# Optimization experiments

Measured on AMD Instinct MI355X. Metric: run time of the kernel, lower is better.

The kernel has to match this reference:

```python
import jax, jax.numpy as jnp
import numpy as np

N_NODES = 100000


def gcn_conv(h_in, W, b, src, dst, ew, n_nodes):
    """PyG GCNConv: x' = D^{-1/2} (A + I) D^{-1/2} (x W) + b, with edge weights."""
    h = h_in @ W  # [N, F_out]
    loop = jnp.arange(n_nodes, dtype=src.dtype)
    row = jnp.concatenate([src, loop])            # sources (j)
    col = jnp.concatenate([dst, loop])            # targets (i)
    w = jnp.concatenate([ew, jnp.ones((n_nodes,), dtype=ew.dtype)])
    deg = jax.ops.segment_sum(w, col, num_segments=n_nodes)  # weighted in-degree incl. self-loops
    dinv = jnp.where(deg > 0, jax.lax.rsqrt(deg), 0.0)
    norm = dinv[row] * w * dinv[col]              # [E+N]
    msg = h[row] * norm[:, None]                  # gather + scale, [E+N, F_out]
    out = jax.ops.segment_sum(msg, col, num_segments=n_nodes)  # scatter to targets
    return out + b


def setup_inputs() -> dict:
    key = jax.random.key(0)
    k = jax.random.split(key, 6)
    N, E, F_in, F_hid = N_NODES, 3200000, 128, 64
    x = jax.random.normal(k[0], (N, F_in), dtype=jnp.float32)
    edge_index = jax.random.randint(k[1], (2, E), 0, N, dtype=jnp.int64)
    edge_weight = jax.random.uniform(k[2], (E,), dtype=jnp.float32)
    W1 = jax.random.normal(k[3], (F_in, F_hid), dtype=jnp.float32) * 0.1
    b1 = jnp.zeros((F_hid,), dtype=jnp.float32)
    W2 = jax.random.normal(k[4], (F_hid, 1), dtype=jnp.float32) * 0.1
    b2 = jnp.zeros((1,), dtype=jnp.float32)
    return {"x": x, "edge_index": edge_index, "edge_weight": edge_weight,
            "W1": W1, "b1": b1, "W2": W2, "b2": b2}


def reference(x, edge_index, edge_weight, W1, b1, W2, b2):
    n_nodes = x.shape[0]
    src, dst = edge_index[0], edge_index[1]
    h = jax.nn.relu(gcn_conv(x, W1, b1, src, dst, edge_weight, n_nodes))
    h = gcn_conv(h, W2, b2, src, dst, edge_weight, n_nodes)  # [N, 1]
    score = jax.nn.sigmoid(h)[:, 0]
    # degree-weighted scoring (original edges, no self-loops), scatter onto source
    deg_weighted = jax.ops.segment_sum(edge_weight, src, num_segments=n_nodes)
    deg_norm = deg_weighted / jnp.max(deg_weighted)
    return score * (1.0 + deg_norm)
```

## Files before the change

### kernel.cpp

```cpp
#include <hip/hip_runtime.h>
#include <hip/hip_fp16.h>
#include <math.h>

#define F_IN 128
#define F_HID 64
#define NWG 256
#define PT 1024
#define BSH 7
#define BSZ 128
#define BSHS 10
#define BSZS 1024
#define SEGCAP 6144

typedef float f32x2 __attribute__((ext_vector_type(2)));
typedef float f32x4 __attribute__((ext_vector_type(4)));
typedef __bf16 bf16x8 __attribute__((ext_vector_type(8)));

__device__ __forceinline__ unsigned char f32_to_fp8(float v) {
  unsigned r = __builtin_amdgcn_cvt_pk_fp8_f32(v, v, 0, false);
  return (unsigned char)(r & 0xFFu);
}

__device__ __forceinline__ __bf16 f32_bf16(float f) {
  unsigned u = __float_as_uint(f);
  unsigned r = (u + 0x7FFFu + ((u >> 16) & 1u)) >> 16;
  return __builtin_bit_cast(__bf16, (unsigned short)r);
}

__global__ void k_count(const int* __restrict__ src, const int* __restrict__ dst,
                        int* __restrict__ cntAll, int NBD, int NBS, int E) {
  extern __shared__ int sh[];
  int* hD = sh;
  int* hS = sh + NBD;
  int tid = threadIdx.x, w = blockIdx.x;
  for (int k = tid; k < NBD + NBS; k += PT) sh[k] = 0;
  __syncthreads();
  int C = (E + NWG - 1) / NWG;
  int e0 = w * C, e1 = min(E, e0 + C);
  for (int e = e0 + tid; e < e1; e += PT) {
    atomicAdd(&hD[dst[e] >> BSH], 1);
    atomicAdd(&hS[src[e] >> BSHS], 1);
  }
  __syncthreads();
  for (int b = tid; b < NBD; b += PT) cntAll[b * NWG + w] = hD[b];
  for (int b = tid; b < NBS; b += PT) cntAll[(NBD + b) * NWG + w] = hS[b];
}

__global__ void k_scanA(int* __restrict__ data, int* __restrict__ partials, int TOT) {
  __shared__ int lds[1024];
  int tid = threadIdx.x;
  int g = blockIdx.x * 1024 + tid;
  int v = (g < TOT) ? data[g] : 0;
  lds[tid] = v; __syncthreads();
  for (int o = 1; o < 1024; o <<= 1) {
    int t = (tid >= o) ? lds[tid - o] : 0;
    __syncthreads();
    lds[tid] += t;
    __syncthreads();
  }
  if (g < TOT) data[g] = lds[tid] - v;
  if (tid == 1023) partials[blockIdx.x] = lds[1023];
}

__global__ void k_scanB(int* partials, int nb, unsigned* maxbits) {
  __shared__ int lds[1024];
  int tid = threadIdx.x;
  if (tid == 0) *maxbits = 0u;
  int v = (tid < nb) ? partials[tid] : 0;
  lds[tid] = v; __syncthreads();
  for (int o = 1; o < 1024; o <<= 1) {
    int t = (tid >= o) ? lds[tid - o] : 0;
    __syncthreads();
    lds[tid] += t;
    __syncthreads();
  }
  if (tid < nb) partials[tid] = lds[tid] - v;
}

__global__ void k_scanC(int* __restrict__ data, const int* __restrict__ partials, int TOT) {
  int g = blockIdx.x * 1024 + threadIdx.x;
  if (g < TOT) data[g] += partials[g >> 10];
}

__global__ void k_part(const int* __restrict__ src, const int* __restrict__ dst,
                       const float* __restrict__ ew, const int* __restrict__ baseAll,
                       int2* __restrict__ gD, unsigned* __restrict__ gS,
                       int NBD, int NBS, int E) {
  extern __shared__ int sh[];
  int* cD = sh;
  int* cS = sh + NBD;
  int tid = threadIdx.x, w = blockIdx.x;
  for (int b = tid; b < NBD; b += PT) cD[b] = baseAll[b * NWG + w];
  for (int b = tid; b < NBS; b += PT) cS[b] = baseAll[(NBD + b) * NWG + w] - E;
  __syncthreads();
  int C = (E + NWG - 1) / NWG;
  int e0 = w * C, e1 = min(E, e0 + C);
  for (int e = e0 + tid; e < e1; e += PT) {
    int s = src[e], d = dst[e];
    float wv = ew[e];
    int pD = atomicAdd(&cD[d >> BSH], 1);
    gD[pD] = make_int2(s | ((d & (BSZ - 1)) << 24), __float_as_int(wv));
    int pS = atomicAdd(&cS[s >> BSHS], 1);
    unsigned hb = (unsigned)__half_as_ushort(__float2half(wv));
    gS[pS] = ((unsigned)(s & (BSZS - 1)) << 16) | hb;
  }
}

__global__ void k_csr(int2* __restrict__ gD, const int* __restrict__ baseAll,
                      int* __restrict__ off, float* __restrict__ dinv,
                      int NBD, int N, int E) {
  __shared__ int2 seg[SEGCAP];
  __shared__ int hist[BSZ];
  __shared__ int curs[BSZ];
  __shared__ float degf[BSZ];
  int tid = threadIdx.x, b = blockIdx.x;
  int bstart = baseAll[b * NWG];
  int bend = (b + 1 < NBD) ? baseAll[(b + 1) * NWG] : E;
  int cnt = bend - bstart;
  for (int k = tid; k < cnt; k += 256) seg[k] = gD[bstart + k];
  if (tid < BSZ) { hist[tid] = 0; degf[tid] = 0.f; }
  __syncthreads();
  for (int k = tid; k < cnt; k += 256) {
    int dl = seg[k].x >> 24;
    atomicAdd(&hist[dl], 1);
    atomicAdd(&degf[dl], __int_as_float(seg[k].y));
  }
  __syncthreads();
  int v = (tid < BSZ) ? hist[tid] : 0;
  for (int o = 1; o < BSZ; o <<= 1) {
    int t = (tid < BSZ && tid >= o) ? hist[tid - o] : 0;
    __syncthreads();
    if (tid < BSZ) hist[tid] += t;
    __syncthreads();
  }
  if (tid < BSZ) {
    int excl = hist[tid] - v;
    curs[tid] = excl;
    int node = b * BSZ + tid;
    if (node < N) {
      off[node] = bstart + excl;
      dinv[node] = rsqrtf(1.0f + degf[tid]);
    }
  }
  if (b == NBD - 1 && tid == 0) off[N] = E;
  __syncthreads();
  for (int k = tid; k < cnt; k += 256) {
    int2 ev = seg[k];
    int dl = ev.x >> 24;
    int slot = atomicAdd(&curs[dl], 1);
    gD[bstart + slot] = make_int2(ev.x & 0xFFFFFF, ev.y);
  }
}

__global__ void k_dw(const unsigned* __restrict__ gS, const int* __restrict__ baseAll,
                     float* __restrict__ dw, unsigned* maxbits,
                     int NBD, int NBS, int N, int E) {
  __shared__ float acc[BSZS];
  int tid = threadIdx.x, b = blockIdx.x;
  int bstart = baseAll[(NBD + b) * NWG] - E;
  int bend = (b + 1 < NBS) ? baseAll[(NBD + b + 1) * NWG] - E : E;
  acc[tid] = 0.f;
  __syncthreads();
  for (int k = bstart + tid; k < bend; k += BSZS) {
    unsigned p = gS[k];
    atomicAdd(&acc[p >> 16], __half2float(__ushort_as_half((unsigned short)(p & 0xFFFFu))));
  }
  __syncthreads();
  float m = 0.f;
  int node = b * BSZS + tid;
  if (node < N) { dw[node] = acc[tid]; m = acc[tid]; }
  for (int mm = 32; mm; mm >>= 1) m = fmaxf(m, __shfl_xor(m, mm, 64));
  if ((tid & 63) == 0) atomicMax(maxbits, __float_as_uint(m));
}

__global__ void k_gemm1(const float* __restrict__ x, const float* __restrict__ W1,
                        const float* __restrict__ dinv, unsigned char* __restrict__ g0, int N) {
  int lane = threadIdx.x & 63;
  int wid = (blockIdx.x * blockDim.x + threadIdx.x) >> 6;
  int nw = (gridDim.x * blockDim.x) >> 6;
  int l16 = lane & 15, lh = lane >> 4;
  bf16x8 bfrag[4][4];
#pragma unroll
  for (int cb = 0; cb < 4; ++cb)
#pragma unroll
    for (int kf = 0; kf < 4; ++kf)
#pragma unroll
      for (int i = 0; i < 8; ++i) {
        int k = kf * 32 + lh * 8 + i;
        bfrag[cb][kf][i] = f32_bf16(W1[k * F_HID + cb * 16 + l16]);
      }
  int ntiles = (N + 15) >> 4;
  for (int t = wid; t < ntiles; t += nw) {
    int rowbase = t << 4;
    int row = min(rowbase + l16, N - 1);
    bf16x8 afrag[4];
#pragma unroll
    for (int kf = 0; kf < 4; ++kf) {
      const f32x4* xp = (const f32x4*)(x + (size_t)row * F_IN + kf * 32 + lh * 8);
      f32x4 v0 = xp[0], v1 = xp[1];
#pragma unroll
      for (int i = 0; i < 4; ++i) afrag[kf][i] = f32_bf16(v0[i]);
#pragma unroll
      for (int i = 0; i < 4; ++i) afrag[kf][4 + i] = f32_bf16(v1[i]);
    }
    f32x4 acc[4] = {{0.f,0.f,0.f,0.f},{0.f,0.f,0.f,0.f},{0.f,0.f,0.f,0.f},{0.f,0.f,0.f,0.f}};
#pragma unroll
    for (int cb = 0; cb < 4; ++cb)
#pragma unroll
      for (int kf = 0; kf < 4; ++kf)
        acc[cb] = __builtin_amdgcn_mfma_f32_16x16x32_bf16(afrag[kf], bfrag[cb][kf], acc[cb], 0, 0, 0);
    if (rowbase + 16 <= N) {
      f32x4 dv = *(const f32x4*)(dinv + rowbase + lh * 4);
#pragma unroll
      for (int cb = 0; cb < 4; ++cb)
#pragma unroll
        for (int r = 0; r < 4; ++r) {
          int rr = rowbase + lh * 4 + r;
          g0[(size_t)rr * F_HID + cb * 16 + l16] = f32_to_fp8(acc[cb][r] * dv[r]);
        }
    } else {
#pragma unroll
      for (int cb = 0; cb < 4; ++cb)
#pragma unroll
        for (int r = 0; r < 4; ++r) {
          int rr = rowbase + lh * 4 + r;
          if (rr < N)
            g0[(size_t)rr * F_HID + cb * 16 + l16] = f32_to_fp8(acc[cb][r] * dinv[rr]);
        }
    }
  }
}

__global__ void k_agg1(const unsigned char* __restrict__ g0, const float* __restrict__ dinv,
                       const int* __restrict__ off, const int2* __restrict__ csr,
                       const float* __restrict__ b1, const float* __restrict__ W2,
                       float* __restrict__ u, int N) {
  int lane = threadIdx.x & 63;
  int grp = lane >> 3;
  int l8  = lane & 7;
  int i = (blockIdx.x * blockDim.x + threadIdx.x) >> 6;
  if (i >= N) return;
  const uint2* g0v = (const uint2*)g0;
  float acc[8] = {0.f, 0.f, 0.f, 0.f, 0.f, 0.f, 0.f, 0.f};
  if (grp == 0) {
    uint2 rv = g0v[(size_t)i * 8 + l8];
    f32x2 c0 = __builtin_amdgcn_cvt_pk_f32_fp8(rv.x, false);
    f32x2 c1 = __builtin_amdgcn_cvt_pk_f32_fp8(rv.x, true);
    f32x2 c2 = __builtin_amdgcn_cvt_pk_f32_fp8(rv.y, false);
    f32x2 c3 = __builtin_amdgcn_cvt_pk_f32_fp8(rv.y, true);
    acc[0] += c0.x; acc[1] += c0.y; acc[2] += c1.x; acc[3] += c1.y;
    acc[4] += c2.x; acc[5] += c2.y; acc[6] += c3.x; acc[7] += c3.y;
  }
  int p0 = off[i], p1 = off[i + 1];
  for (int p = p0; p < p1; p += 64) {
    int m = min(p1 - p, 64);
    int2 ed = make_int2(0, 0);
    if (lane < m) ed = csr[p + lane];
#pragma unroll
    for (int jj = 0; jj < 8; ++jj) {
      int j = jj * 8 + grp;
      int s = __shfl(ed.x, j, 64);
      float w = __int_as_float(__shfl(ed.y, j, 64));
      if (j < m) {
        uint2 rv = g0v[(size_t)s * 8 + l8];
        f32x2 c0 = __builtin_amdgcn_cvt_pk_f32_fp8(rv.x, false);
        f32x2 c1 = __builtin_amdgcn_cvt_pk_f32_fp8(rv.x, true);
        f32x2 c2 = __builtin_amdgcn_cvt_pk_f32_fp8(rv.y, false);
        f32x2 c3 = __builtin_amdgcn_cvt_pk_f32_fp8(rv.y, true);
        acc[0] = fmaf(w, c0.x, acc[0]); acc[1] = fmaf(w, c0.y, acc[1]);
        acc[2] = fmaf(w, c1.x, acc[2]); acc[3] = fmaf(w, c1.y, acc[3]);
        acc[4] = fmaf(w, c2.x, acc[4]); acc[5] = fmaf(w, c2.y, acc[5]);
        acc[6] = fmaf(w, c3.x, acc[6]); acc[7] = fmaf(w, c3.y, acc[7]);
      }
    }
  }
#pragma unroll
  for (int k = 0; k < 8; ++k) {
    acc[k] += __shfl_xor(acc[k], 8, 64);
    acc[k] += __shfl_xor(acc[k], 16, 64);
    acc[k] += __shfl_xor(acc[k], 32, 64);
  }
  float di = dinv[i];
  float pdt = 0.f;
#pragma unroll
  for (int k = 0; k < 8; ++k) {
    int f = l8 * 8 + k;
    float h = fmaxf(di * acc[k] + b1[f], 0.f);
    pdt = fmaf(h, W2[f], pdt);
  }
  pdt += __shfl_xor(pdt, 1, 64);
  pdt += __shfl_xor(pdt, 2, 64);
  pdt += __shfl_xor(pdt, 4, 64);
  if (lane == 0) u[i] = di * pdt;
}

__global__ void k_agg2_final(const float* __restrict__ u, const float* __restrict__ dinv,
                             const int* __restrict__ off, const int2* __restrict__ csr,
                             const float* __restrict__ b2, const float* __restrict__ dw,
                             const unsigned* __restrict__ maxbits,
                             float* __restrict__ out, int N) {
  int lane32 = threadIdx.x & 31;
  int i = blockIdx.x * 8 + (threadIdx.x >> 5);
  if (i >= N) return;
  float acc = (lane32 == 0) ? u[i] : 0.f;
  int p0 = off[i], p1 = off[i + 1];
  for (int p = p0 + lane32; p < p1; p += 32) {
    int2 ed = csr[p];
    acc = fmaf(__int_as_float(ed.y), u[ed.x], acc);
  }
  for (int mm = 16; mm; mm >>= 1) acc += __shfl_xor(acc, mm, 64);
  if (lane32 == 0) {
    float md = __uint_as_float(*maxbits);
    float z = dinv[i] * acc + b2[0];
    float sc = 1.0f / (1.0f + expf(-z));
    out[i] = sc * (1.0f + dw[i] / md);
  }
}

extern "C" void kernel_launch(void* const* d_in, const int* in_sizes, int n_in,
                              void* d_out, int out_size, void* d_ws, size_t ws_size,
                              hipStream_t stream) {
  const float* x  = (const float*)d_in[0];
  const int*   ei = (const int*)d_in[1];
  const float* ew = (const float*)d_in[2];
  const float* W1 = (const float*)d_in[3];
  const float* b1 = (const float*)d_in[4];
  const float* W2 = (const float*)d_in[5];
  const float* b2 = (const float*)d_in[6];
  float* out = (float*)d_out;

  int N = out_size;
  int E = in_sizes[2];
  const int* src = ei;
  const int* dst = ei + E;

  int NBD = (N + BSZ - 1) >> BSH;
  int NBS = (N + BSZS - 1) >> BSHS;
  int TOT = (NBD + NBS) * NWG;
  int SB = (TOT + 1023) >> 10;
  size_t shmem = (size_t)(NBD + NBS) * sizeof(int);

  char* w8 = (char*)d_ws;
  int2*     gD      = (int2*)w8;
  unsigned* gS      = (unsigned*)(gD + E);
  int*      cntAll  = (int*)(gS + E);
  int*      partials= cntAll + TOT;
  int*      off     = partials + 1024;
  float*    dinv    = (float*)(off + N + 1);
  float*    dw      = dinv + N;
  float*    u       = dw + N;
  unsigned* maxbits = (unsigned*)(u + N);
  unsigned char* g0 = (unsigned char*)(maxbits + 2);

  k_count<<<NWG, PT, shmem, stream>>>(src, dst, cntAll, NBD, NBS, E);
  k_scanA<<<SB, 1024, 0, stream>>>(cntAll, partials, TOT);
  k_scanB<<<1, 1024, 0, stream>>>(partials, SB, maxbits);
  k_scanC<<<SB, 1024, 0, stream>>>(cntAll, partials, TOT);
  k_part<<<NWG, PT, shmem, stream>>>(src, dst, ew, cntAll, gD, gS, NBD, NBS, E);
  k_csr<<<NBD, 256, 0, stream>>>(gD, cntAll, off, dinv, NBD, N, E);
  k_dw<<<NBS, BSZS, 0, stream>>>(gS, cntAll, dw, maxbits, NBD, NBS, N, E);
  k_gemm1<<<256, 256, 0, stream>>>(x, W1, dinv, g0, N);
  k_agg1<<<(N * 64 + 255) / 256, 256, 0, stream>>>(g0, dinv, off, gD, b1, W2, u, N);
  k_agg2_final<<<(N + 7) / 8, 256, 0, stream>>>(u, dinv, off, gD, b2, dw, maxbits, out, N);
}
```

Baseline: 270.5 us.

## Replace scan-based partition with slab-allocated buckets and atomic cursors

Removes the separate counting pass and three-kernel prefix scan by giving each 1024-node bucket a fixed-capacity slab in workspace, with per-block offsets claimed by global atomics. CSR build now runs one 1024-thread block per bucket and writes into a separate array, storing per-node degree instead of an end offset. Nontemporal loads are added for streaming reads of x, edge weights and CSR entries. Fixed slab capacity assumes a roughly uniform number of edges per bucket and would overflow on skewed graphs.

```diff
diff --git a/kernel.cpp b/kernel.cpp
--- a/kernel.cpp
+++ b/kernel.cpp
@@ -6,11 +6,7 @@
 #define F_HID 64
 #define NWG 256
 #define PT 1024
-#define BSH 7
-#define BSZ 128
-#define BSHS 10
-#define BSZS 1024
-#define SEGCAP 6144
+#define SLAB 36864
 
 typedef float f32x2 __attribute__((ext_vector_type(2)));
 typedef float f32x4 __attribute__((ext_vector_type(4)));
@@ -27,147 +23,107 @@
   return __builtin_bit_cast(__bf16, (unsigned short)r);
 }
 
-__global__ void k_count(const int* __restrict__ src, const int* __restrict__ dst,
-                        int* __restrict__ cntAll, int NBD, int NBS, int E) {
-  extern __shared__ int sh[];
-  int* hD = sh;
-  int* hS = sh + NBD;
+__device__ __forceinline__ int2 nt_i2(const int2* p) {
+  long long v = __builtin_nontemporal_load((const long long*)p);
+  return make_int2((int)(v & 0xFFFFFFFFll), (int)(v >> 32));
+}
+
+__global__ void k_init0(int* cursD, int* cursS, unsigned* maxbits, int nbc) {
+  int t = threadIdx.x;
+  if (t < nbc) { cursD[t] = t * SLAB; cursS[t] = t * SLAB; }
+  if (t == 0) *maxbits = 0u;
+}
+
+__global__ void k_partA(const int* __restrict__ src, const int* __restrict__ dst,
+                        const float* __restrict__ ew, int* cursD, int* cursS,
+                        int2* __restrict__ gDc, unsigned* __restrict__ gS,
+                        int nbc, int E) {
+  __shared__ int hD[128], hS[128];
   int tid = threadIdx.x, w = blockIdx.x;
-  for (int k = tid; k < NBD + NBS; k += PT) sh[k] = 0;
+  if (tid < 128) { hD[tid] = 0; hS[tid] = 0; }
   __syncthreads();
   int C = (E + NWG - 1) / NWG;
   int e0 = w * C, e1 = min(E, e0 + C);
   for (int e = e0 + tid; e < e1; e += PT) {
-    atomicAdd(&hD[dst[e] >> BSH], 1);
-    atomicAdd(&hS[src[e] >> BSHS], 1);
-  }
-  __syncthreads();
-  for (int b = tid; b < NBD; b += PT) cntAll[b * NWG + w] = hD[b];
-  for (int b = tid; b < NBS; b += PT) cntAll[(NBD + b) * NWG + w] = hS[b];
-}
-
-__global__ void k_scanA(int* __restrict__ data, int* __restrict__ partials, int TOT) {
-  __shared__ int lds[1024];
-  int tid = threadIdx.x;
-  int g = blockIdx.x * 1024 + tid;
-  int v = (g < TOT) ? data[g] : 0;
-  lds[tid] = v; __syncthreads();
-  for (int o = 1; o < 1024; o <<= 1) {
-    int t = (tid >= o) ? lds[tid - o] : 0;
-    __syncthreads();
-    lds[tid] += t;
-    __syncthreads();
-  }
-  if (g < TOT) data[g] = lds[tid] - v;
-  if (tid == 1023) partials[blockIdx.x] = lds[1023];
-}
-
-__global__ void k_scanB(int* partials, int nb, unsigned* maxbits) {
-  __shared__ int lds[1024];
-  int tid = threadIdx.x;
-  if (tid == 0) *maxbits = 0u;
-  int v = (tid < nb) ? partials[tid] : 0;
-  lds[tid] = v; __syncthreads();
-  for (int o = 1; o < 1024; o <<= 1) {
-    int t = (tid >= o) ? lds[tid - o] : 0;
-    __syncthreads();
-    lds[tid] += t;
-    __syncthreads();
-  }
-  if (tid < nb) partials[tid] = lds[tid] - v;
-}
-
-__global__ void k_scanC(int* __restrict__ data, const int* __restrict__ partials, int TOT) {
-  int g = blockIdx.x * 1024 + threadIdx.x;
-  if (g < TOT) data[g] += partials[g >> 10];
-}
-
-__global__ void k_part(const int* __restrict__ src, const int* __restrict__ dst,
-                       const float* __restrict__ ew, const int* __restrict__ baseAll,
-                       int2* __restrict__ gD, unsigned* __restrict__ gS,
-                       int NBD, int NBS, int E) {
-  extern __shared__ int sh[];
-  int* cD = sh;
-  int* cS = sh + NBD;
-  int tid = threadIdx.x, w = blockIdx.x;
-  for (int b = tid; b < NBD; b += PT) cD[b] = baseAll[b * NWG + w];
-  for (int b = tid; b < NBS; b += PT) cS[b] = baseAll[(NBD + b) * NWG + w] - E;
-  __syncthreads();
-  int C = (E + NWG - 1) / NWG;
-  int e0 = w * C, e1 = min(E, e0 + C);
+    atomicAdd(&hD[dst[e] >> 10], 1);
+    atomicAdd(&hS[src[e] >> 10], 1);
+  }
+  __syncthreads();
+  if (tid < nbc) {
+    int c = hD[tid];
+    hD[tid] = c ? atomicAdd(&cursD[tid], c) : 0;
+  } else if (tid < 2 * nbc) {
+    int b = tid - nbc;
+    int c = hS[b];
+    hS[b] = c ? atomicAdd(&cursS[b], c) : 0;
+  }
+  __syncthreads();
   for (int e = e0 + tid; e < e1; e += PT) {
     int s = src[e], d = dst[e];
-    float wv = ew[e];
-    int pD = atomicAdd(&cD[d >> BSH], 1);
-    gD[pD] = make_int2(s | ((d & (BSZ - 1)) << 24), __float_as_int(wv));
-    int pS = atomicAdd(&cS[s >> BSHS], 1);
-    unsigned hb = (unsigned)__half_as_ushort(__float2half(wv));
-    gS[pS] = ((unsigned)(s & (BSZS - 1)) << 16) | hb;
-  }
-}
-
-__global__ void k_csr(int2* __restrict__ gD, const int* __restrict__ baseAll,
-                      int* __restrict__ off, float* __restrict__ dinv,
-                      int NBD, int N, int E) {
-  __shared__ int2 seg[SEGCAP];
-  __shared__ int hist[BSZ];
-  __shared__ int curs[BSZ];
-  __shared__ float degf[BSZ];
+    float wv = __builtin_nontemporal_load(&ew[e]);
+    int pD = atomicAdd(&hD[d >> 10], 1);
+    gDc[pD] = make_int2(s | ((d & 1023) << 17), __float_as_int(wv));
+    int pS = atomicAdd(&hS[s >> 10], 1);
+    gS[pS] = ((unsigned)(s & 1023) << 16) | (unsigned)__half_as_ushort(__float2half(wv));
+  }
+}
+
+__global__ void k_build(const int2* __restrict__ gDc, const int* __restrict__ cursD,
+                        int2* __restrict__ csrE, int* __restrict__ off,
+                        int* __restrict__ degN, float* __restrict__ dinv,
+                        int nbc, int N) {
+  __shared__ int hist[1024];
+  __shared__ float degf[1024];
+  __shared__ int curs[1024];
+  int tid = threadIdx.x, bc = blockIdx.x;
+  int cstart = bc * SLAB, cend = cursD[bc];
+  hist[tid] = 0; degf[tid] = 0.f;
+  __syncthreads();
+  for (int k = cstart + tid; k < cend; k += 1024) {
+    int2 ev = gDc[k];
+    int dl = (ev.x >> 17) & 1023;
+    atomicAdd(&hist[dl], 1);
+    atomicAdd(&degf[dl], __int_as_float(ev.y));
+  }
+  __syncthreads();
+  int v = hist[tid];
+  for (int o = 1; o < 1024; o <<= 1) {
+    int t = (tid >= o) ? hist[tid - o] : 0;
+    __syncthreads();
+    hist[tid] += t;
+    __syncthreads();
+  }
+  int excl = hist[tid] - v;
+  curs[tid] = cstart + excl;
+  int node = bc * 1024 + tid;
+  if (node < N) {
+    off[node] = cstart + excl;
+    degN[node] = v;
+    dinv[node] = rsqrtf(1.0f + degf[tid]);
+  }
+  __syncthreads();
+  for (int k = cstart + tid; k < cend; k += 1024) {
+    int2 ev = gDc[k];
+    int dl = (ev.x >> 17) & 1023;
+    int p = atomicAdd(&curs[dl], 1);
+    csrE[p] = make_int2(ev.x & 0x1FFFF, ev.y);
+  }
+}
+
+__global__ void k_dw(const unsigned* __restrict__ gS, const int* __restrict__ cursS,
+                     float* __restrict__ dw, unsigned* maxbits, int nbc, int N) {
+  __shared__ float acc[1024];
   int tid = threadIdx.x, b = blockIdx.x;
-  int bstart = baseAll[b * NWG];
-  int bend = (b + 1 < NBD) ? baseAll[(b + 1) * NWG] : E;
-  int cnt = bend - bstart;
-  for (int k = tid; k < cnt; k += 256) seg[k] = gD[bstart + k];
-  if (tid < BSZ) { hist[tid] = 0; degf[tid] = 0.f; }
-  __syncthreads();
-  for (int k = tid; k < cnt; k += 256) {
-    int dl = seg[k].x >> 24;
-    atomicAdd(&hist[dl], 1);
-    atomicAdd(&degf[dl], __int_as_float(seg[k].y));
-  }
-  __syncthreads();
-  int v = (tid < BSZ) ? hist[tid] : 0;
-  for (int o = 1; o < BSZ; o <<= 1) {
-    int t = (tid < BSZ && tid >= o) ? hist[tid - o] : 0;
-    __syncthreads();
-    if (tid < BSZ) hist[tid] += t;
-    __syncthreads();
-  }
-  if (tid < BSZ) {
-    int excl = hist[tid] - v;
-    curs[tid] = excl;
-    int node = b * BSZ + tid;
-    if (node < N) {
-      off[node] = bstart + excl;
-      dinv[node] = rsqrtf(1.0f + degf[tid]);
-    }
-  }
-  if (b == NBD - 1 && tid == 0) off[N] = E;
-  __syncthreads();
-  for (int k = tid; k < cnt; k += 256) {
-    int2 ev = seg[k];
-    int dl = ev.x >> 24;
-    int slot = atomicAdd(&curs[dl], 1);
-    gD[bstart + slot] = make_int2(ev.x & 0xFFFFFF, ev.y);
-  }
-}
-
-__global__ void k_dw(const unsigned* __restrict__ gS, const int* __restrict__ baseAll,
-                     float* __restrict__ dw, unsigned* maxbits,
-                     int NBD, int NBS, int N, int E) {
-  __shared__ float acc[BSZS];
-  int tid = threadIdx.x, b = blockIdx.x;
-  int bstart = baseAll[(NBD + b) * NWG] - E;
-  int bend = (b + 1 < NBS) ? baseAll[(NBD + b + 1) * NWG] - E : E;
+  int bstart = b * SLAB, bend = cursS[b];
   acc[tid] = 0.f;
   __syncthreads();
-  for (int k = bstart + tid; k < bend; k += BSZS) {
-    unsigned p = gS[k];
+  for (int k = bstart + tid; k < bend; k += 1024) {
+    unsigned p = __builtin_nontemporal_load(&gS[k]);
     atomicAdd(&acc[p >> 16], __half2float(__ushort_as_half((unsigned short)(p & 0xFFFFu))));
   }
   __syncthreads();
   float m = 0.f;
-  int node = b * BSZS + tid;
+  int node = b * 1024 + tid;
   if (node < N) { dw[node] = acc[tid]; m = acc[tid]; }
   for (int mm = 32; mm; mm >>= 1) m = fmaxf(m, __shfl_xor(m, mm, 64));
   if ((tid & 63) == 0) atomicMax(maxbits, __float_as_uint(m));
@@ -197,7 +153,8 @@
 #pragma unroll
     for (int kf = 0; kf < 4; ++kf) {
       const f32x4* xp = (const f32x4*)(x + (size_t)row * F_IN + kf * 32 + lh * 8);
-      f32x4 v0 = xp[0], v1 = xp[1];
+      f32x4 v0 = __builtin_nontemporal_load(xp);
+      f32x4 v1 = __builtin_nontemporal_load(xp + 1);
 #pragma unroll
       for (int i = 0; i < 4; ++i) afrag[kf][i] = f32_bf16(v0[i]);
 #pragma unroll
@@ -232,7 +189,8 @@
 }
 
 __global__ void k_agg1(const unsigned char* __restrict__ g0, const float* __restrict__ dinv,
-                       const int* __restrict__ off, const int2* __restrict__ csr,
+                       const int* __restrict__ off, const int* __restrict__ degN,
+                       const int2* __restrict__ csr,
                        const float* __restrict__ b1, const float* __restrict__ W2,
                        float* __restrict__ u, int N) {
   int lane = threadIdx.x & 63;
@@ -251,11 +209,11 @@
     acc[0] += c0.x; acc[1] += c0.y; acc[2] += c1.x; acc[3] += c1.y;
     acc[4] += c2.x; acc[5] += c2.y; acc[6] += c3.x; acc[7] += c3.y;
   }
-  int p0 = off[i], p1 = off[i + 1];
+  int p0 = off[i], p1 = p0 + degN[i];
   for (int p = p0; p < p1; p += 64) {
     int m = min(p1 - p, 64);
     int2 ed = make_int2(0, 0);
-    if (lane < m) ed = csr[p + lane];
+    if (lane < m) ed = nt_i2(&csr[p + lane]);
 #pragma unroll
     for (int jj = 0; jj < 8; ++jj) {
       int j = jj * 8 + grp;
@@ -295,7 +253,8 @@
 }
 
 __global__ void k_agg2_final(const float* __restrict__ u, const float* __restrict__ dinv,
-                             const int* __restrict__ off, const int2* __restrict__ csr,
+                             const int* __restrict__ off, const int* __restrict__ degN,
+                             const int2* __restrict__ csr,
                              const float* __restrict__ b2, const float* __restrict__ dw,
                              const unsigned* __restrict__ maxbits,
                              float* __restrict__ out, int N) {
@@ -303,9 +262,9 @@
   int i = blockIdx.x * 8 + (threadIdx.x >> 5);
   if (i >= N) return;
   float acc = (lane32 == 0) ? u[i] : 0.f;
-  int p0 = off[i], p1 = off[i + 1];
+  int p0 = off[i], p1 = p0 + degN[i];
   for (int p = p0 + lane32; p < p1; p += 32) {
-    int2 ed = csr[p];
+    int2 ed = nt_i2(&csr[p]);
     acc = fmaf(__int_as_float(ed.y), u[ed.x], acc);
   }
   for (int mm = 16; mm; mm >>= 1) acc += __shfl_xor(acc, mm, 64);
@@ -334,32 +293,28 @@
   const int* src = ei;
   const int* dst = ei + E;
 
-  int NBD = (N + BSZ - 1) >> BSH;
-  int NBS = (N + BSZS - 1) >> BSHS;
-  int TOT = (NBD + NBS) * NWG;
-  int SB = (TOT + 1023) >> 10;
-  size_t shmem = (size_t)(NBD + NBS) * sizeof(int);
+  int nbc = (N + 1023) >> 10;
+  size_t slabTot = (size_t)nbc * SLAB;
 
   char* w8 = (char*)d_ws;
-  int2*     gD      = (int2*)w8;
-  unsigned* gS      = (unsigned*)(gD + E);
-  int*      cntAll  = (int*)(gS + E);
-  int*      partials= cntAll + TOT;
-  int*      off     = partials + 1024;
-  float*    dinv    = (float*)(off + N + 1);
-  float*    dw      = dinv + N;
-  float*    u       = dw + N;
+  int2*     gDc   = (int2*)w8;
+  int2*     csrE  = gDc + slabTot;
+  unsigned* gS    = (unsigned*)(csrE + slabTot);
+  int*      cursD = (int*)(gS + slabTot);
+  int*      cursS = cursD + nbc;
+  int*      off   = cursS + nbc;
+  int*      degN  = off + N;
+  float*    dinv  = (float*)(degN + N);
+  float*    dw    = dinv + N;
+  float*    u     = dw + N;
   unsigned* maxbits = (unsigned*)(u + N);
-  unsigned char* g0 = (unsigned char*)(maxbits + 2);
-
-  k_count<<<NWG, PT, shmem, stream>>>(src, dst, cntAll, NBD, NBS, E);
-  k_scanA<<<SB, 1024, 0, stream>>>(cntAll, partials, TOT);
-  k_scanB<<<1, 1024, 0, stream>>>(partials, SB, maxbits);
-  k_scanC<<<SB, 1024, 0, stream>>>(cntAll, partials, TOT);
-  k_part<<<NWG, PT, shmem, stream>>>(src, dst, ew, cntAll, gD, gS, NBD, NBS, E);
-  k_csr<<<NBD, 256, 0, stream>>>(gD, cntAll, off, dinv, NBD, N, E);
-  k_dw<<<NBS, BSZS, 0, stream>>>(gS, cntAll, dw, maxbits, NBD, NBS, N, E);
+  unsigned char* g0 = (unsigned char*)(maxbits + 4);
+
+  k_init0<<<1, 128, 0, stream>>>(cursD, cursS, maxbits, nbc);
+  k_partA<<<NWG, PT, 0, stream>>>(src, dst, ew, cursD, cursS, gDc, gS, nbc, E);
+  k_build<<<nbc, 1024, 0, stream>>>(gDc, cursD, csrE, off, degN, dinv, nbc, N);
+  k_dw<<<nbc, 1024, 0, stream>>>(gS, cursS, dw, maxbits, nbc, N);
   k_gemm1<<<256, 256, 0, stream>>>(x, W1, dinv, g0, N);
-  k_agg1<<<(N * 64 + 255) / 256, 256, 0, stream>>>(g0, dinv, off, gD, b1, W2, u, N);
-  k_agg2_final<<<(N + 7) / 8, 256, 0, stream>>>(u, dinv, off, gD, b2, dw, maxbits, out, N);
-}
+  k_agg1<<<(N * 64 + 255) / 256, 256, 0, stream>>>(g0, dinv, off, degN, csrE, b1, W2, u, N);
+  k_agg2_final<<<(N + 7) / 8, 256, 0, stream>>>(u, dinv, off, degN, csrE, b2, dw, maxbits, out, N);
+}
```

Result: slower. 327.3 us (+21.0%).

## Fuse CSR sort into aggregation kernel via LDS, scatter-add layer two

Applied to the files above, without the earlier changes.

The separate k_csr pass, which sorted each destination bucket and wrote the sorted edges back to global memory, is removed. k_deg now only computes the histogram, offsets, per-node degree and dinv. The first aggregation runs one 1024-thread block per 128-node bucket: it sorts the bucket's edges into LDS and aggregates directly from there. The second layer uses per-bucket shared-memory atomic scatter over the unsorted edges instead of a CSR gather. This removes a global read/write pass over the edges but cuts parallelism in agg1 (one block per 128 nodes, fixed 8 nodes per wave) and relies on each bucket fitting in SEGCAP.

```diff
diff --git a/kernel.cpp b/kernel.cpp
--- a/kernel.cpp
+++ b/kernel.cpp
@@ -101,29 +101,25 @@
     int pD = atomicAdd(&cD[d >> BSH], 1);
     gD[pD] = make_int2(s | ((d & (BSZ - 1)) << 24), __float_as_int(wv));
     int pS = atomicAdd(&cS[s >> BSHS], 1);
-    unsigned hb = (unsigned)__half_as_ushort(__float2half(wv));
-    gS[pS] = ((unsigned)(s & (BSZS - 1)) << 16) | hb;
-  }
-}
-
-__global__ void k_csr(int2* __restrict__ gD, const int* __restrict__ baseAll,
-                      int* __restrict__ off, float* __restrict__ dinv,
-                      int NBD, int N, int E) {
-  __shared__ int2 seg[SEGCAP];
+    gS[pS] = ((unsigned)(s & (BSZS - 1)) << 16) | (unsigned)__half_as_ushort(__float2half(wv));
+  }
+}
+
+__global__ void k_deg(const int2* __restrict__ gD, const int* __restrict__ baseAll,
+                      int* __restrict__ off, int* __restrict__ degN,
+                      float* __restrict__ dinv, int NBD, int N, int E) {
   __shared__ int hist[BSZ];
-  __shared__ int curs[BSZ];
   __shared__ float degf[BSZ];
   int tid = threadIdx.x, b = blockIdx.x;
   int bstart = baseAll[b * NWG];
   int bend = (b + 1 < NBD) ? baseAll[(b + 1) * NWG] : E;
-  int cnt = bend - bstart;
-  for (int k = tid; k < cnt; k += 256) seg[k] = gD[bstart + k];
   if (tid < BSZ) { hist[tid] = 0; degf[tid] = 0.f; }
   __syncthreads();
-  for (int k = tid; k < cnt; k += 256) {
-    int dl = seg[k].x >> 24;
+  for (int k = bstart + tid; k < bend; k += 256) {
+    int2 ev = gD[k];
+    int dl = (unsigned)ev.x >> 24;
     atomicAdd(&hist[dl], 1);
-    atomicAdd(&degf[dl], __int_as_float(seg[k].y));
+    atomicAdd(&degf[dl], __int_as_float(ev.y));
   }
   __syncthreads();
   int v = (tid < BSZ) ? hist[tid] : 0;
@@ -134,21 +130,12 @@
     __syncthreads();
   }
   if (tid < BSZ) {
-    int excl = hist[tid] - v;
-    curs[tid] = excl;
     int node = b * BSZ + tid;
     if (node < N) {
-      off[node] = bstart + excl;
+      off[node] = bstart + (hist[tid] - v);
+      degN[node] = v;
       dinv[node] = rsqrtf(1.0f + degf[tid]);
     }
-  }
-  if (b == NBD - 1 && tid == 0) off[N] = E;
-  __syncthreads();
-  for (int k = tid; k < cnt; k += 256) {
-    int2 ev = seg[k];
-    int dl = ev.x >> 24;
-    int slot = atomicAdd(&curs[dl], 1);
-    gD[bstart + slot] = make_int2(ev.x & 0xFFFFFF, ev.y);
   }
 }
 
@@ -231,89 +218,117 @@
   }
 }
 
-__global__ void k_agg1(const unsigned char* __restrict__ g0, const float* __restrict__ dinv,
-                       const int* __restrict__ off, const int2* __restrict__ csr,
-                       const float* __restrict__ b1, const float* __restrict__ W2,
-                       float* __restrict__ u, int N) {
-  int lane = threadIdx.x & 63;
-  int grp = lane >> 3;
-  int l8  = lane & 7;
-  int i = (blockIdx.x * blockDim.x + threadIdx.x) >> 6;
-  if (i >= N) return;
+__global__ void __launch_bounds__(1024) k_agg1m(
+    const unsigned char* __restrict__ g0, const float* __restrict__ dinv,
+    const int* __restrict__ baseAll, const int* __restrict__ off,
+    const int* __restrict__ degN, const int2* __restrict__ gD,
+    const float* __restrict__ b1, const float* __restrict__ W2,
+    float* __restrict__ u, int NBD, int N, int E) {
+  __shared__ int2 seg[SEGCAP];
+  __shared__ int curs[BSZ];
+  int tid = threadIdx.x, b = blockIdx.x;
+  int bstart = baseAll[b * NWG];
+  int bend = (b + 1 < NBD) ? baseAll[(b + 1) * NWG] : E;
+  if (tid < BSZ) {
+    int node = b * BSZ + tid;
+    curs[tid] = (node < N) ? (off[node] - bstart) : 0;
+  }
+  __syncthreads();
+  for (int k = bstart + tid; k < bend; k += 1024) {
+    int2 ev = gD[k];
+    int dl = (unsigned)ev.x >> 24;
+    int slot = atomicAdd(&curs[dl], 1);
+    seg[slot] = make_int2(ev.x & 0xFFFFFF, ev.y);
+  }
+  __syncthreads();
+  int lane = tid & 63;
+  int wv = tid >> 6;
+  int grp = lane >> 3, l8 = lane & 7;
   const uint2* g0v = (const uint2*)g0;
-  float acc[8] = {0.f, 0.f, 0.f, 0.f, 0.f, 0.f, 0.f, 0.f};
-  if (grp == 0) {
-    uint2 rv = g0v[(size_t)i * 8 + l8];
-    f32x2 c0 = __builtin_amdgcn_cvt_pk_f32_fp8(rv.x, false);
-    f32x2 c1 = __builtin_amdgcn_cvt_pk_f32_fp8(rv.x, true);
-    f32x2 c2 = __builtin_amdgcn_cvt_pk_f32_fp8(rv.y, false);
-    f32x2 c3 = __builtin_amdgcn_cvt_pk_f32_fp8(rv.y, true);
-    acc[0] += c0.x; acc[1] += c0.y; acc[2] += c1.x; acc[3] += c1.y;
-    acc[4] += c2.x; acc[5] += c2.y; acc[6] += c3.x; acc[7] += c3.y;
-  }
-  int p0 = off[i], p1 = off[i + 1];
-  for (int p = p0; p < p1; p += 64) {
-    int m = min(p1 - p, 64);
-    int2 ed = make_int2(0, 0);
-    if (lane < m) ed = csr[p + lane];
-#pragma unroll
-    for (int jj = 0; jj < 8; ++jj) {
-      int j = jj * 8 + grp;
-      int s = __shfl(ed.x, j, 64);
-      float w = __int_as_float(__shfl(ed.y, j, 64));
-      if (j < m) {
-        uint2 rv = g0v[(size_t)s * 8 + l8];
-        f32x2 c0 = __builtin_amdgcn_cvt_pk_f32_fp8(rv.x, false);
-        f32x2 c1 = __builtin_amdgcn_cvt_pk_f32_fp8(rv.x, true);
-        f32x2 c2 = __builtin_amdgcn_cvt_pk_f32_fp8(rv.y, false);
-        f32x2 c3 = __builtin_amdgcn_cvt_pk_f32_fp8(rv.y, true);
-        acc[0] = fmaf(w, c0.x, acc[0]); acc[1] = fmaf(w, c0.y, acc[1]);
-        acc[2] = fmaf(w, c1.x, acc[2]); acc[3] = fmaf(w, c1.y, acc[3]);
-        acc[4] = fmaf(w, c2.x, acc[4]); acc[5] = fmaf(w, c2.y, acc[5]);
-        acc[6] = fmaf(w, c3.x, acc[6]); acc[7] = fmaf(w, c3.y, acc[7]);
+  float b1v[8], w2v[8];
+#pragma unroll
+  for (int k = 0; k < 8; ++k) { b1v[k] = b1[l8 * 8 + k]; w2v[k] = W2[l8 * 8 + k]; }
+  for (int n = wv * 8; n < wv * 8 + 8; ++n) {
+    int node = b * BSZ + n;
+    if (node >= N) break;
+    float acc[8] = {0.f, 0.f, 0.f, 0.f, 0.f, 0.f, 0.f, 0.f};
+    if (grp == 0) {
+      uint2 rv = g0v[(size_t)node * 8 + l8];
+      f32x2 c0 = __builtin_amdgcn_cvt_pk_f32_fp8(rv.x, false);
+      f32x2 c1 = __builtin_amdgcn_cvt_pk_f32_fp8(rv.x, true);
+      f32x2 c2 = __builtin_amdgcn_cvt_pk_f32_fp8(rv.y, false);
+      f32x2 c3 = __builtin_amdgcn_cvt_pk_f32_fp8(rv.y, true);
+      acc[0] += c0.x; acc[1] += c0.y; acc[2] += c1.x; acc[3] += c1.y;
+      acc[4] += c2.x; acc[5] += c2.y; acc[6] += c3.x; acc[7] += c3.y;
+    }
+    int p0 = off[node] - bstart;
+    int dn = degN[node];
+    for (int p = 0; p < dn; p += 64) {
+      int m = min(dn - p, 64);
+      int2 ed = make_int2(0, 0);
+      if (lane < m) ed = seg[p0 + p + lane];
+#pragma unroll
+      for (int jj = 0; jj < 8; ++jj) {
+        int j = jj * 8 + grp;
+        int s = __shfl(ed.x, j, 64);
+        float w = __int_as_float(__shfl(ed.y, j, 64));
+        if (j < m) {
+          uint2 rv = g0v[(size_t)s * 8 + l8];
+          f32x2 c0 = __builtin_amdgcn_cvt_pk_f32_fp8(rv.x, false);
+          f32x2 c1 = __builtin_amdgcn_cvt_pk_f32_fp8(rv.x, true);
+          f32x2 c2 = __builtin_amdgcn_cvt_pk_f32_fp8(rv.y, false);
+          f32x2 c3 = __builtin_amdgcn_cvt_pk_f32_fp8(rv.y, true);
+          acc[0] = fmaf(w, c0.x, acc[0]); acc[1] = fmaf(w, c0.y, acc[1]);
+          acc[2] = fmaf(w, c1.x, acc[2]); acc[3] = fmaf(w, c1.y, acc[3]);
+          acc[4] = fmaf(w, c2.x, acc[4]); acc[5] = fmaf(w, c2.y, acc[5]);
+          acc[6] = fmaf(w, c3.x, acc[6]); acc[7] = fmaf(w, c3.y, acc[7]);
+        }
       }
     }
-  }
-#pragma unroll
-  for (int k = 0; k < 8; ++k) {
-    acc[k] += __shfl_xor(acc[k], 8, 64);
-    acc[k] += __shfl_xor(acc[k], 16, 64);
-    acc[k] += __shfl_xor(acc[k], 32, 64);
-  }
-  float di = dinv[i];
-  float pdt = 0.f;
-#pragma unroll
-  for (int k = 0; k < 8; ++k) {
-    int f = l8 * 8 + k;
-    float h = fmaxf(di * acc[k] + b1[f], 0.f);
-    pdt = fmaf(h, W2[f], pdt);
-  }
-  pdt += __shfl_xor(pdt, 1, 64);
-  pdt += __shfl_xor(pdt, 2, 64);
-  pdt += __shfl_xor(pdt, 4, 64);
-  if (lane == 0) u[i] = di * pdt;
-}
-
-__global__ void k_agg2_final(const float* __restrict__ u, const float* __restrict__ dinv,
-                             const int* __restrict__ off, const int2* __restrict__ csr,
-                             const float* __restrict__ b2, const float* __restrict__ dw,
-                             const unsigned* __restrict__ maxbits,
-                             float* __restrict__ out, int N) {
-  int lane32 = threadIdx.x & 31;
-  int i = blockIdx.x * 8 + (threadIdx.x >> 5);
-  if (i >= N) return;
-  float acc = (lane32 == 0) ? u[i] : 0.f;
-  int p0 = off[i], p1 = off[i + 1];
-  for (int p = p0 + lane32; p < p1; p += 32) {
-    int2 ed = csr[p];
-    acc = fmaf(__int_as_float(ed.y), u[ed.x], acc);
-  }
-  for (int mm = 16; mm; mm >>= 1) acc += __shfl_xor(acc, mm, 64);
-  if (lane32 == 0) {
-    float md = __uint_as_float(*maxbits);
-    float z = dinv[i] * acc + b2[0];
-    float sc = 1.0f / (1.0f + expf(-z));
-    out[i] = sc * (1.0f + dw[i] / md);
+#pragma unroll
+    for (int k = 0; k < 8; ++k) {
+      acc[k] += __shfl_xor(acc[k], 8, 64);
+      acc[k] += __shfl_xor(acc[k], 16, 64);
+      acc[k] += __shfl_xor(acc[k], 32, 64);
+    }
+    float di = dinv[node];
+    float pdt = 0.f;
+#pragma unroll
+    for (int k = 0; k < 8; ++k) {
+      float h = fmaxf(di * acc[k] + b1v[k], 0.f);
+      pdt = fmaf(h, w2v[k], pdt);
+    }
+    pdt += __shfl_xor(pdt, 1, 64);
+    pdt += __shfl_xor(pdt, 2, 64);
+    pdt += __shfl_xor(pdt, 4, 64);
+    if (lane == 0) u[node] = di * pdt;
+  }
+}
+
+__global__ void k_agg2s(const float* __restrict__ u, const float* __restrict__ dinv,
+                        const int* __restrict__ baseAll, const int2* __restrict__ gD,
+                        const float* __restrict__ b2, const float* __restrict__ dw,
+                        const unsigned* __restrict__ maxbits,
+                        float* __restrict__ out, int NBD, int N, int E) {
+  __shared__ float acc[BSZ];
+  int tid = threadIdx.x, b = blockIdx.x;
+  int bstart = baseAll[b * NWG];
+  int bend = (b + 1 < NBD) ? baseAll[(b + 1) * NWG] : E;
+  if (tid < BSZ) acc[tid] = 0.f;
+  __syncthreads();
+  for (int k = bstart + tid; k < bend; k += 256) {
+    int2 ev = gD[k];
+    atomicAdd(&acc[(unsigned)ev.x >> 24], __int_as_float(ev.y) * u[ev.x & 0xFFFFFF]);
+  }
+  __syncthreads();
+  if (tid < BSZ) {
+    int node = b * BSZ + tid;
+    if (node < N) {
+      float md = __uint_as_float(*maxbits);
+      float z = dinv[node] * (u[node] + acc[tid]) + b2[0];
+      float sc = 1.0f / (1.0f + expf(-z));
+      out[node] = sc * (1.0f + dw[node] / md);
+    }
   }
 }
 
@@ -346,20 +361,21 @@
   int*      cntAll  = (int*)(gS + E);
   int*      partials= cntAll + TOT;
   int*      off     = partials + 1024;
-  float*    dinv    = (float*)(off + N + 1);
+  int*      degN    = off + N;
+  float*    dinv    = (float*)(degN + N);
   float*    dw      = dinv + N;
   float*    u       = dw + N;
   unsigned* maxbits = (unsigned*)(u + N);
-  unsigned char* g0 = (unsigned char*)(maxbits + 2);
+  unsigned char* g0 = (unsigned char*)(maxbits + 4);
 
   k_count<<<NWG, PT, shmem, stream>>>(src, dst, cntAll, NBD, NBS, E);
   k_scanA<<<SB, 1024, 0, stream>>>(cntAll, partials, TOT);
   k_scanB<<<1, 1024, 0, stream>>>(partials, SB, maxbits);
   k_scanC<<<SB, 1024, 0, stream>>>(cntAll, partials, TOT);
   k_part<<<NWG, PT, shmem, stream>>>(src, dst, ew, cntAll, gD, gS, NBD, NBS, E);
-  k_csr<<<NBD, 256, 0, stream>>>(gD, cntAll, off, dinv, NBD, N, E);
+  k_deg<<<NBD, 256, 0, stream>>>(gD, cntAll, off, degN, dinv, NBD, N, E);
   k_dw<<<NBS, BSZS, 0, stream>>>(gS, cntAll, dw, maxbits, NBD, NBS, N, E);
   k_gemm1<<<256, 256, 0, stream>>>(x, W1, dinv, g0, N);
-  k_agg1<<<(N * 64 + 255) / 256, 256, 0, stream>>>(g0, dinv, off, gD, b1, W2, u, N);
-  k_agg2_final<<<(N + 7) / 8, 256, 0, stream>>>(u, dinv, off, gD, b2, dw, maxbits, out, N);
-}
+  k_agg1m<<<NBD, 1024, 0, stream>>>(g0, dinv, cntAll, off, degN, gD, b1, W2, u, NBD, N, E);
+  k_agg2s<<<NBD, 256, 0, stream>>>(u, dinv, cntAll, gD, b2, dw, maxbits, out, NBD, N, E);
+}
```

Result: slower. 302.2 us (+11.7%).

## Split layer-1 aggregation into two feature halves for cache-resident gathers

Applied to the files above, without the earlier changes.

The GEMM now writes the fp8 hidden features as two separate 32-column arrays, and the layer-1 aggregation runs twice, once per half, so each gathered table is about 3.2 MB and more likely to stay in L2/MALL during random neighbor gathers. Because ReLU and the W2 dot product are per-feature, the first pass stores its partial dot product and the second pass adds it and applies dinv. CSR edge loads also use nontemporal hints. The cost is reading the CSR edge list twice and launching one extra kernel.

```diff
diff --git a/kernel.cpp b/kernel.cpp
--- a/kernel.cpp
+++ b/kernel.cpp
@@ -25,6 +25,11 @@
   unsigned u = __float_as_uint(f);
   unsigned r = (u + 0x7FFFu + ((u >> 16) & 1u)) >> 16;
   return __builtin_bit_cast(__bf16, (unsigned short)r);
+}
+
+__device__ __forceinline__ int2 nt_i2(const int2* p) {
+  long long v = __builtin_nontemporal_load((const long long*)p);
+  return make_int2((int)(v & 0xFFFFFFFFll), (int)(v >> 32));
 }
 
 __global__ void k_count(const int* __restrict__ src, const int* __restrict__ dst,
@@ -101,8 +106,7 @@
     int pD = atomicAdd(&cD[d >> BSH], 1);
     gD[pD] = make_int2(s | ((d & (BSZ - 1)) << 24), __float_as_int(wv));
     int pS = atomicAdd(&cS[s >> BSHS], 1);
-    unsigned hb = (unsigned)__half_as_ushort(__float2half(wv));
-    gS[pS] = ((unsigned)(s & (BSZS - 1)) << 16) | hb;
+    gS[pS] = ((unsigned)(s & (BSZS - 1)) << 16) | (unsigned)__half_as_ushort(__float2half(wv));
   }
 }
 
@@ -121,7 +125,7 @@
   if (tid < BSZ) { hist[tid] = 0; degf[tid] = 0.f; }
   __syncthreads();
   for (int k = tid; k < cnt; k += 256) {
-    int dl = seg[k].x >> 24;
+    int dl = (unsigned)seg[k].x >> 24;
     atomicAdd(&hist[dl], 1);
     atomicAdd(&degf[dl], __int_as_float(seg[k].y));
   }
@@ -146,7 +150,7 @@
   __syncthreads();
   for (int k = tid; k < cnt; k += 256) {
     int2 ev = seg[k];
-    int dl = ev.x >> 24;
+    int dl = (unsigned)ev.x >> 24;
     int slot = atomicAdd(&curs[dl], 1);
     gD[bstart + slot] = make_int2(ev.x & 0xFFFFFF, ev.y);
   }
@@ -174,7 +178,8 @@
 }
 
 __global__ void k_gemm1(const float* __restrict__ x, const float* __restrict__ W1,
-                        const float* __restrict__ dinv, unsigned char* __restrict__ g0, int N) {
+                        const float* __restrict__ dinv,
+                        unsigned char* __restrict__ g0a, unsigned char* __restrict__ g0b, int N) {
   int lane = threadIdx.x & 63;
   int wid = (blockIdx.x * blockDim.x + threadIdx.x) >> 6;
   int nw = (gridDim.x * blockDim.x) >> 6;
@@ -209,41 +214,34 @@
 #pragma unroll
       for (int kf = 0; kf < 4; ++kf)
         acc[cb] = __builtin_amdgcn_mfma_f32_16x16x32_bf16(afrag[kf], bfrag[cb][kf], acc[cb], 0, 0, 0);
-    if (rowbase + 16 <= N) {
-      f32x4 dv = *(const f32x4*)(dinv + rowbase + lh * 4);
-#pragma unroll
-      for (int cb = 0; cb < 4; ++cb)
-#pragma unroll
-        for (int r = 0; r < 4; ++r) {
-          int rr = rowbase + lh * 4 + r;
-          g0[(size_t)rr * F_HID + cb * 16 + l16] = f32_to_fp8(acc[cb][r] * dv[r]);
-        }
-    } else {
-#pragma unroll
-      for (int cb = 0; cb < 4; ++cb)
-#pragma unroll
-        for (int r = 0; r < 4; ++r) {
-          int rr = rowbase + lh * 4 + r;
-          if (rr < N)
-            g0[(size_t)rr * F_HID + cb * 16 + l16] = f32_to_fp8(acc[cb][r] * dinv[rr]);
-        }
+#pragma unroll
+    for (int cb = 0; cb < 4; ++cb) {
+      unsigned char* dstp = (cb < 2) ? g0a : g0b;
+      int fl = (cb & 1) * 16 + l16;
+#pragma unroll
+      for (int r = 0; r < 4; ++r) {
+        int rr = rowbase + lh * 4 + r;
+        if (rr < N)
+          dstp[(size_t)rr * 32 + fl] = f32_to_fp8(acc[cb][r] * dinv[rr]);
+      }
     }
   }
 }
 
-__global__ void k_agg1(const unsigned char* __restrict__ g0, const float* __restrict__ dinv,
-                       const int* __restrict__ off, const int2* __restrict__ csr,
-                       const float* __restrict__ b1, const float* __restrict__ W2,
-                       float* __restrict__ u, int N) {
+__global__ void k_agg1h(const unsigned char* __restrict__ g0h, const float* __restrict__ dinv,
+                        const int* __restrict__ off, const int2* __restrict__ csr,
+                        const float* __restrict__ b1h, const float* __restrict__ W2h,
+                        float* __restrict__ upart, float* __restrict__ u,
+                        int finalPass, int N) {
   int lane = threadIdx.x & 63;
-  int grp = lane >> 3;
-  int l8  = lane & 7;
+  int grp = lane >> 2;
+  int l4  = lane & 3;
   int i = (blockIdx.x * blockDim.x + threadIdx.x) >> 6;
   if (i >= N) return;
-  const uint2* g0v = (const uint2*)g0;
+  const uint2* g0v = (const uint2*)g0h;
   float acc[8] = {0.f, 0.f, 0.f, 0.f, 0.f, 0.f, 0.f, 0.f};
   if (grp == 0) {
-    uint2 rv = g0v[(size_t)i * 8 + l8];
+    uint2 rv = g0v[(size_t)i * 4 + l4];
     f32x2 c0 = __builtin_amdgcn_cvt_pk_f32_fp8(rv.x, false);
     f32x2 c1 = __builtin_amdgcn_cvt_pk_f32_fp8(rv.x, true);
     f32x2 c2 = __builtin_amdgcn_cvt_pk_f32_fp8(rv.y, false);
@@ -255,14 +253,14 @@
   for (int p = p0; p < p1; p += 64) {
     int m = min(p1 - p, 64);
     int2 ed = make_int2(0, 0);
-    if (lane < m) ed = csr[p + lane];
-#pragma unroll
-    for (int jj = 0; jj < 8; ++jj) {
-      int j = jj * 8 + grp;
+    if (lane < m) ed = nt_i2(&csr[p + lane]);
+#pragma unroll
+    for (int jj = 0; jj < 4; ++jj) {
+      int j = jj * 16 + grp;
       int s = __shfl(ed.x, j, 64);
       float w = __int_as_float(__shfl(ed.y, j, 64));
       if (j < m) {
-        uint2 rv = g0v[(size_t)s * 8 + l8];
+        uint2 rv = g0v[(size_t)s * 4 + l4];
         f32x2 c0 = __builtin_amdgcn_cvt_pk_f32_fp8(rv.x, false);
         f32x2 c1 = __builtin_amdgcn_cvt_pk_f32_fp8(rv.x, true);
         f32x2 c2 = __builtin_amdgcn_cvt_pk_f32_fp8(rv.y, false);
@@ -276,6 +274,7 @@
   }
 #pragma unroll
   for (int k = 0; k < 8; ++k) {
+    acc[k] += __shfl_xor(acc[k], 4, 64);
     acc[k] += __shfl_xor(acc[k], 8, 64);
     acc[k] += __shfl_xor(acc[k], 16, 64);
     acc[k] += __shfl_xor(acc[k], 32, 64);
@@ -284,14 +283,16 @@
   float pdt = 0.f;
 #pragma unroll
   for (int k = 0; k < 8; ++k) {
-    int f = l8 * 8 + k;
-    float h = fmaxf(di * acc[k] + b1[f], 0.f);
-    pdt = fmaf(h, W2[f], pdt);
+    int f = l4 * 8 + k;
+    float h = fmaxf(di * acc[k] + b1h[f], 0.f);
+    pdt = fmaf(h, W2h[f], pdt);
   }
   pdt += __shfl_xor(pdt, 1, 64);
   pdt += __shfl_xor(pdt, 2, 64);
-  pdt += __shfl_xor(pdt, 4, 64);
-  if (lane == 0) u[i] = di * pdt;
+  if (lane == 0) {
+    if (finalPass) u[i] = di * (upart[i] + pdt);
+    else upart[i] = pdt;
+  }
 }
 
 __global__ void k_agg2_final(const float* __restrict__ u, const float* __restrict__ dinv,
@@ -306,7 +307,7 @@
   int p0 = off[i], p1 = off[i + 1];
   for (int p = p0 + lane32; p < p1; p += 32) {
     int2 ed = csr[p];
-    acc = fmaf(__int_as_float(ed.y), u[ed.x], acc);
+    acc = fmaf(__int_as_float(ed.y), u[ed.x & 0xFFFFFF], acc);
   }
   for (int mm = 16; mm; mm >>= 1) acc += __shfl_xor(acc, mm, 64);
   if (lane32 == 0) {
@@ -349,8 +350,10 @@
   float*    dinv    = (float*)(off + N + 1);
   float*    dw      = dinv + N;
   float*    u       = dw + N;
-  unsigned* maxbits = (unsigned*)(u + N);
-  unsigned char* g0 = (unsigned char*)(maxbits + 2);
+  float*    upart   = u + N;
+  unsigned* maxbits = (unsigned*)(upart + N);
+  unsigned char* g0a = (unsigned char*)(maxbits + 4);
+  unsigned char* g0b = g0a + (size_t)N * 32;
 
   k_count<<<NWG, PT, shmem, stream>>>(src, dst, cntAll, NBD, NBS, E);
   k_scanA<<<SB, 1024, 0, stream>>>(cntAll, partials, TOT);
@@ -359,7 +362,8 @@
   k_part<<<NWG, PT, shmem, stream>>>(src, dst, ew, cntAll, gD, gS, NBD, NBS, E);
   k_csr<<<NBD, 256, 0, stream>>>(gD, cntAll, off, dinv, NBD, N, E);
   k_dw<<<NBS, BSZS, 0, stream>>>(gS, cntAll, dw, maxbits, NBD, NBS, N, E);
-  k_gemm1<<<256, 256, 0, stream>>>(x, W1, dinv, g0, N);
-  k_agg1<<<(N * 64 + 255) / 256, 256, 0, stream>>>(g0, dinv, off, gD, b1, W2, u, N);
+  k_gemm1<<<256, 256, 0, stream>>>(x, W1, dinv, g0a, g0b, N);
+  k_agg1h<<<(N * 64 + 255) / 256, 256, 0, stream>>>(g0a, dinv, off, gD, b1, W2, upart, u, 0, N);
+  k_agg1h<<<(N * 64 + 255) / 256, 256, 0, stream>>>(g0b, dinv, off, gD, b1 + 32, W2 + 32, upart, u, 1, N);
   k_agg2_final<<<(N + 7) / 8, 256, 0, stream>>>(u, dinv, off, gD, b2, dw, maxbits, out, N);
 }
```

Result: slower. 333.6 us (+23.3%).
